# Kernel optimization log

Measured on AMD Instinct MI355X. Metric: run time of the kernel, lower is better.

## Reference

```python
import jax, jax.numpy as jnp
import numpy as np

N1 = 4097
N2 = 8192


def setup_inputs() -> dict:
    key = jax.random.key(0)
    kx, ka, kb, km = jax.random.split(key, 4)
    x = jax.random.normal(kx, ((N1 - 1) * N2 + 1,), dtype=jnp.float32)
    a = jax.random.uniform(ka, (1,), dtype=jnp.float32)
    b = jax.random.uniform(kb, (N2, N1 - 1), dtype=jnp.float32)
    mu = jax.random.uniform(km, (1,), dtype=jnp.float32)
    return {"x": x, "a": a, "b": b, "mu": mu}


def reference(x, a, b, mu):
    n2, n1m1 = b.shape  # (n2, n1-1)
    n1 = n1m1 + 1
    # y = x[1 : (n1-1)*n2 + 1].reshape(n2, n1-1)
    y = x[1:(n1 - 1) * n2 + 1].reshape(n2, n1 - 1)
    # Original loop: i in range(n1-2), j in range(n2-1); term uses y[j, i-1],
    # which at i=0 wraps to the LAST column (negative indexing). Reproduce via roll.
    y_cur = y[: n2 - 1, : n1 - 2]                       # y[j, i]
    y_prev = jnp.roll(y, 1, axis=1)[: n2 - 1, : n1 - 2]  # y[j, i-1] with wraparound
    terms = b[: n2 - 1, : n1 - 2] * (y_cur - y_prev ** 2) ** 2
    return -a * (x[0] - mu) ** 2 - jnp.sum(terms)
```

## Files before the change

kernel.cpp:

```cpp
#include <hip/hip_runtime.h>


#define ROWS  8191
#define BLOCK 256

__global__ __launch_bounds__(BLOCK) void rosen_partial(
    const float* __restrict__ x, const float* __restrict__ b,
    float* __restrict__ partial)
{
    const unsigned r = blockIdx.x;
    const unsigned t = threadIdx.x;
    const size_t   e = (size_t)r * 4096u + (size_t)t * 16u;

    const float4* __restrict__ x4 = (const float4*)(x + e);
    const float4* __restrict__ b4 = (const float4*)(b + e);

    float4 xv0 = x4[0], xv1 = x4[1], xv2 = x4[2], xv3 = x4[3];
    float4 bv0 = b4[0], bv1 = b4[1], bv2 = b4[2], bv3 = b4[3];
    float  xs  = x[e + 16];

    float p0 = (t == 0) ? x[e + 4096] : xv0.x;
    if (t == BLOCK - 1) bv3.w = 0.0f;

    float d, acc;
    d = xv0.y - p0    * p0;     acc  = bv0.x * d * d;
    d = xv0.z - xv0.y * xv0.y;  acc += bv0.y * d * d;
    d = xv0.w - xv0.z * xv0.z;  acc += bv0.z * d * d;
    d = xv1.x - xv0.w * xv0.w;  acc += bv0.w * d * d;
    d = xv1.y - xv1.x * xv1.x;  acc += bv1.x * d * d;
    d = xv1.z - xv1.y * xv1.y;  acc += bv1.y * d * d;
    d = xv1.w - xv1.z * xv1.z;  acc += bv1.z * d * d;
    d = xv2.x - xv1.w * xv1.w;  acc += bv1.w * d * d;
    d = xv2.y - xv2.x * xv2.x;  acc += bv2.x * d * d;
    d = xv2.z - xv2.y * xv2.y;  acc += bv2.y * d * d;
    d = xv2.w - xv2.z * xv2.z;  acc += bv2.z * d * d;
    d = xv3.x - xv2.w * xv2.w;  acc += bv2.w * d * d;
    d = xv3.y - xv3.x * xv3.x;  acc += bv3.x * d * d;
    d = xv3.z - xv3.y * xv3.y;  acc += bv3.y * d * d;
    d = xv3.w - xv3.z * xv3.z;  acc += bv3.z * d * d;
    d = xs    - xv3.w * xv3.w;  acc += bv3.w * d * d;

    #pragma unroll
    for (int off = 32; off > 0; off >>= 1)
        acc += __shfl_down(acc, off, 64);

    __shared__ float s[4];
    const int lane = t & 63;
    const int wid  = t >> 6;
    if (lane == 0) s[wid] = acc;
    __syncthreads();
    if (t == 0)
        partial[r] = s[0] + s[1] + s[2] + s[3];
}

__global__ __launch_bounds__(256) void rosen_final(const float* __restrict__ partial,
                                                   const float* __restrict__ x,
                                                   const float* __restrict__ a,
                                                   const float* __restrict__ mu,
                                                   float* __restrict__ out)
{
    float acc = 0.0f;
    for (int i = threadIdx.x; i < ROWS; i += 256)
        acc += partial[i];

    #pragma unroll
    for (int off = 32; off > 0; off >>= 1)
        acc += __shfl_down(acc, off, 64);

    __shared__ float s[4];
    const int lane = threadIdx.x & 63;
    const int wid  = threadIdx.x >> 6;
    if (lane == 0) s[wid] = acc;
    __syncthreads();
    if (threadIdx.x == 0) {
        float total = s[0] + s[1] + s[2] + s[3];
        float dd = x[0] - mu[0];
        out[0] = -a[0] * dd * dd - total;
    }
}

extern "C" void kernel_launch(void* const* d_in, const int* in_sizes, int n_in,
                              void* d_out, int out_size, void* d_ws, size_t ws_size,
                              hipStream_t stream) {
    const float* x  = (const float*)d_in[0];
    const float* a  = (const float*)d_in[1];
    const float* b  = (const float*)d_in[2];
    const float* mu = (const float*)d_in[3];
    float* out     = (float*)d_out;
    float* partial = (float*)d_ws;

    rosen_partial<<<ROWS, BLOCK, 0, stream>>>(x, b, partial);
    rosen_final<<<1, 256, 0, stream>>>(partial, x, a, mu, out);
}
```

Before: 284.4 us.

## Use a fixed grid with four batched groups per thread

Replaces the one-block-per-row launch (8191 blocks) with 2048 blocks, where each thread covers four 16-element groups spread out by a grid stride. All loads for the four groups are issued before any compute, so more memory requests are in flight per thread. The final reduction shrinks to 2048 partials. In exchange, register use rises (about 128 floats of loads per thread) and occupancy may drop. Each group now needs its own boundary and validity checks.

```diff
diff --git a/kernel.cpp b/kernel.cpp
--- a/kernel.cpp
+++ b/kernel.cpp
@@ -1,56 +1,88 @@
 #include <hip/hip_runtime.h>
 
 
-#define ROWS  8191
-#define BLOCK 256
+#define ROWS     8191u
+#define GROUPS16 (ROWS * 256u)
+#define GRID     2048
+#define BLOCK    256
+#define NTHREAD  ((unsigned)GRID * BLOCK)
+#define ITERS    4
+
+__device__ __forceinline__ float group16(const float4* xv, const float4* bv,
+                                         float p0, float xs, float bw3)
+{
+    float d, s;
+    d = xv[0].y - p0      * p0;       s  = bv[0].x * d * d;
+    d = xv[0].z - xv[0].y * xv[0].y;  s += bv[0].y * d * d;
+    d = xv[0].w - xv[0].z * xv[0].z;  s += bv[0].z * d * d;
+    d = xv[1].x - xv[0].w * xv[0].w;  s += bv[0].w * d * d;
+    d = xv[1].y - xv[1].x * xv[1].x;  s += bv[1].x * d * d;
+    d = xv[1].z - xv[1].y * xv[1].y;  s += bv[1].y * d * d;
+    d = xv[1].w - xv[1].z * xv[1].z;  s += bv[1].z * d * d;
+    d = xv[2].x - xv[1].w * xv[1].w;  s += bv[1].w * d * d;
+    d = xv[2].y - xv[2].x * xv[2].x;  s += bv[2].x * d * d;
+    d = xv[2].z - xv[2].y * xv[2].y;  s += bv[2].y * d * d;
+    d = xv[2].w - xv[2].z * xv[2].z;  s += bv[2].z * d * d;
+    d = xv[3].x - xv[2].w * xv[2].w;  s += bv[2].w * d * d;
+    d = xv[3].y - xv[3].x * xv[3].x;  s += bv[3].x * d * d;
+    d = xv[3].z - xv[3].y * xv[3].y;  s += bv[3].y * d * d;
+    d = xv[3].w - xv[3].z * xv[3].z;  s += bv[3].z * d * d;
+    d = xs      - xv[3].w * xv[3].w;  s += bw3     * d * d;
+    return s;
+}
 
 __global__ __launch_bounds__(BLOCK) void rosen_partial(
     const float* __restrict__ x, const float* __restrict__ b,
     float* __restrict__ partial)
 {
-    const unsigned r = blockIdx.x;
-    const unsigned t = threadIdx.x;
-    const size_t   e = (size_t)r * 4096u + (size_t)t * 16u;
+    const unsigned tid = blockIdx.x * BLOCK + threadIdx.x;
 
-    const float4* __restrict__ x4 = (const float4*)(x + e);
-    const float4* __restrict__ b4 = (const float4*)(b + e);
+    float4   xv[ITERS][4];
+    float4   bv[ITERS][4];
+    float    xs[ITERS];
+    float    xw[ITERS];
+    unsigned c16a[ITERS];
+    bool     vld[ITERS];
 
-    float4 xv0 = x4[0], xv1 = x4[1], xv2 = x4[2], xv3 = x4[3];
-    float4 bv0 = b4[0], bv1 = b4[1], bv2 = b4[2], bv3 = b4[3];
-    float  xs  = x[e + 16];
+    #pragma unroll
+    for (int it = 0; it < ITERS; ++it) {
+        unsigned g  = tid + (unsigned)it * NTHREAD;
+        bool     v  = (g < GROUPS16);
+        unsigned gc = v ? g : (GROUPS16 - 1u);
+        unsigned c16 = gc & 255u;
+        unsigned e   = (gc >> 8) * 4096u + c16 * 16u;
+        vld[it]  = v;
+        c16a[it] = c16;
+        const float4* x4 = (const float4*)(x + e);
+        const float4* b4 = (const float4*)(b + e);
+        xv[it][0] = x4[0]; xv[it][1] = x4[1]; xv[it][2] = x4[2]; xv[it][3] = x4[3];
+        bv[it][0] = b4[0]; bv[it][1] = b4[1]; bv[it][2] = b4[2]; bv[it][3] = b4[3];
+        xs[it] = x[e + 16];
+        float w = 0.0f;
+        if (c16 == 0u) w = x[e + 4096];
+        xw[it] = w;
+    }
 
-    float p0 = (t == 0) ? x[e + 4096] : xv0.x;
-    if (t == BLOCK - 1) bv3.w = 0.0f;
-
-    float d, acc;
-    d = xv0.y - p0    * p0;     acc  = bv0.x * d * d;
-    d = xv0.z - xv0.y * xv0.y;  acc += bv0.y * d * d;
-    d = xv0.w - xv0.z * xv0.z;  acc += bv0.z * d * d;
-    d = xv1.x - xv0.w * xv0.w;  acc += bv0.w * d * d;
-    d = xv1.y - xv1.x * xv1.x;  acc += bv1.x * d * d;
-    d = xv1.z - xv1.y * xv1.y;  acc += bv1.y * d * d;
-    d = xv1.w - xv1.z * xv1.z;  acc += bv1.z * d * d;
-    d = xv2.x - xv1.w * xv1.w;  acc += bv1.w * d * d;
-    d = xv2.y - xv2.x * xv2.x;  acc += bv2.x * d * d;
-    d = xv2.z - xv2.y * xv2.y;  acc += bv2.y * d * d;
-    d = xv2.w - xv2.z * xv2.z;  acc += bv2.z * d * d;
-    d = xv3.x - xv2.w * xv2.w;  acc += bv2.w * d * d;
-    d = xv3.y - xv3.x * xv3.x;  acc += bv3.x * d * d;
-    d = xv3.z - xv3.y * xv3.y;  acc += bv3.y * d * d;
-    d = xv3.w - xv3.z * xv3.z;  acc += bv3.z * d * d;
-    d = xs    - xv3.w * xv3.w;  acc += bv3.w * d * d;
+    float acc = 0.0f;
+    #pragma unroll
+    for (int it = 0; it < ITERS; ++it) {
+        float p0  = (c16a[it] == 0u)   ? xw[it] : xv[it][0].x;
+        float bw3 = (c16a[it] == 255u) ? 0.0f   : bv[it][3].w;
+        float s = group16(&xv[it][0], &bv[it][0], p0, xs[it], bw3);
+        acc += vld[it] ? s : 0.0f;
+    }
 
     #pragma unroll
     for (int off = 32; off > 0; off >>= 1)
         acc += __shfl_down(acc, off, 64);
 
-    __shared__ float s[4];
-    const int lane = t & 63;
-    const int wid  = t >> 6;
-    if (lane == 0) s[wid] = acc;
+    __shared__ float sred[4];
+    const int lane = threadIdx.x & 63;
+    const int wid  = threadIdx.x >> 6;
+    if (lane == 0) sred[wid] = acc;
     __syncthreads();
-    if (t == 0)
-        partial[r] = s[0] + s[1] + s[2] + s[3];
+    if (threadIdx.x == 0)
+        partial[blockIdx.x] = sred[0] + sred[1] + sred[2] + sred[3];
 }
 
 __global__ __launch_bounds__(256) void rosen_final(const float* __restrict__ partial,
@@ -60,20 +92,20 @@
                                                    float* __restrict__ out)
 {
     float acc = 0.0f;
-    for (int i = threadIdx.x; i < ROWS; i += 256)
+    for (int i = threadIdx.x; i < GRID; i += 256)
         acc += partial[i];
 
     #pragma unroll
     for (int off = 32; off > 0; off >>= 1)
         acc += __shfl_down(acc, off, 64);
 
-    __shared__ float s[4];
+    __shared__ float sred[4];
     const int lane = threadIdx.x & 63;
     const int wid  = threadIdx.x >> 6;
-    if (lane == 0) s[wid] = acc;
+    if (lane == 0) sred[wid] = acc;
     __syncthreads();
     if (threadIdx.x == 0) {
-        float total = s[0] + s[1] + s[2] + s[3];
+        float total = sred[0] + sred[1] + sred[2] + sred[3];
         float dd = x[0] - mu[0];
         out[0] = -a[0] * dd * dd - total;
     }
@@ -89,6 +121,6 @@
     float* out     = (float*)d_out;
     float* partial = (float*)d_ws;
 
-    rosen_partial<<<ROWS, BLOCK, 0, stream>>>(x, b, partial);
+    rosen_partial<<<GRID, BLOCK, 0, stream>>>(x, b, partial);
     rosen_final<<<1, 256, 0, stream>>>(partial, x, a, mu, out);
 }
```

Result: faster. 278.7 us (-2.0%).

## Coalesce row loads with lane-strided float4 and loop four rows per block

Applied to the files above, without the earlier changes.

Each wave now loads contiguous float4 chunks across lanes (stride 4 floats per lane) instead of each thread reading 16 contiguous floats, so global accesses are fully coalesced. Neighbor elements across chunk boundaries are obtained via wave shuffles. Each block processes four rows in a loop, cutting the grid from 8191 to 2048 blocks and shrinking the final reduction. The cost is extra shuffle traffic and boundary handling logic, plus less parallelism per row.

```diff
diff --git a/kernel.cpp b/kernel.cpp
--- a/kernel.cpp
+++ b/kernel.cpp
@@ -1,56 +1,80 @@
 #include <hip/hip_runtime.h>
 
 
-#define ROWS  8191
-#define BLOCK 256
+#define ROWS   8191u
+#define GRID   2048
+#define BLOCK  256
+#define ROWSPB 4u
 
 __global__ __launch_bounds__(BLOCK) void rosen_partial(
     const float* __restrict__ x, const float* __restrict__ b,
     float* __restrict__ partial)
 {
-    const unsigned r = blockIdx.x;
-    const unsigned t = threadIdx.x;
-    const size_t   e = (size_t)r * 4096u + (size_t)t * 16u;
+    const unsigned lane = threadIdx.x & 63u;
+    const unsigned w    = threadIdx.x >> 6;
+    float acc = 0.0f;
 
-    const float4* __restrict__ x4 = (const float4*)(x + e);
-    const float4* __restrict__ b4 = (const float4*)(b + e);
+    #pragma unroll 1
+    for (unsigned k = 0; k < ROWSPB; ++k) {
+        const unsigned r = blockIdx.x * ROWSPB + k;
+        if (r >= ROWS) break;
+        const size_t rowoff = (size_t)r * 4096u;
+        const size_t base   = rowoff + w * 1024u + lane * 4u;
 
-    float4 xv0 = x4[0], xv1 = x4[1], xv2 = x4[2], xv3 = x4[3];
-    float4 bv0 = b4[0], bv1 = b4[1], bv2 = b4[2], bv3 = b4[3];
-    float  xs  = x[e + 16];
+        float4 xv0 = *(const float4*)(x + base);
+        float4 xv1 = *(const float4*)(x + base + 256);
+        float4 xv2 = *(const float4*)(x + base + 512);
+        float4 xv3 = *(const float4*)(x + base + 768);
+        float4 bv0 = *(const float4*)(b + base);
+        float4 bv1 = *(const float4*)(b + base + 256);
+        float4 bv2 = *(const float4*)(b + base + 512);
+        float4 bv3 = *(const float4*)(b + base + 768);
 
-    float p0 = (t == 0) ? x[e + 4096] : xv0.x;
-    if (t == BLOCK - 1) bv3.w = 0.0f;
+        float tail = x[rowoff + w * 1024u + 1024u];
+        float wrapv = 0.0f;
+        if (threadIdx.x == 0) wrapv = x[rowoff + 4096u];
+        if (threadIdx.x == BLOCK - 1) bv3.w = 0.0f;
 
-    float d, acc;
-    d = xv0.y - p0    * p0;     acc  = bv0.x * d * d;
-    d = xv0.z - xv0.y * xv0.y;  acc += bv0.y * d * d;
-    d = xv0.w - xv0.z * xv0.z;  acc += bv0.z * d * d;
-    d = xv1.x - xv0.w * xv0.w;  acc += bv0.w * d * d;
-    d = xv1.y - xv1.x * xv1.x;  acc += bv1.x * d * d;
-    d = xv1.z - xv1.y * xv1.y;  acc += bv1.y * d * d;
-    d = xv1.w - xv1.z * xv1.z;  acc += bv1.z * d * d;
-    d = xv2.x - xv1.w * xv1.w;  acc += bv1.w * d * d;
-    d = xv2.y - xv2.x * xv2.x;  acc += bv2.x * d * d;
-    d = xv2.z - xv2.y * xv2.y;  acc += bv2.y * d * d;
-    d = xv2.w - xv2.z * xv2.z;  acc += bv2.z * d * d;
-    d = xv3.x - xv2.w * xv2.w;  acc += bv2.w * d * d;
-    d = xv3.y - xv3.x * xv3.x;  acc += bv3.x * d * d;
-    d = xv3.z - xv3.y * xv3.y;  acc += bv3.y * d * d;
-    d = xv3.w - xv3.z * xv3.z;  acc += bv3.z * d * d;
-    d = xs    - xv3.w * xv3.w;  acc += bv3.w * d * d;
+        float n0 = __shfl_down(xv0.x, 1, 64);
+        float n1 = __shfl_down(xv1.x, 1, 64);
+        float n2 = __shfl_down(xv2.x, 1, 64);
+        float n3 = __shfl_down(xv3.x, 1, 64);
+        float c1 = __shfl(xv1.x, 0, 64);
+        float c2 = __shfl(xv2.x, 0, 64);
+        float c3 = __shfl(xv3.x, 0, 64);
+        if (lane == 63u) { n0 = c1; n1 = c2; n2 = c3; n3 = tail; }
+
+        float pv = xv0.x;
+        if (threadIdx.x == 0) pv = wrapv;
+
+        float d;
+        d = xv0.y - pv    * pv;     acc += bv0.x * d * d;
+        d = xv0.z - xv0.y * xv0.y;  acc += bv0.y * d * d;
+        d = xv0.w - xv0.z * xv0.z;  acc += bv0.z * d * d;
+        d = n0    - xv0.w * xv0.w;  acc += bv0.w * d * d;
+        d = xv1.y - xv1.x * xv1.x;  acc += bv1.x * d * d;
+        d = xv1.z - xv1.y * xv1.y;  acc += bv1.y * d * d;
+        d = xv1.w - xv1.z * xv1.z;  acc += bv1.z * d * d;
+        d = n1    - xv1.w * xv1.w;  acc += bv1.w * d * d;
+        d = xv2.y - xv2.x * xv2.x;  acc += bv2.x * d * d;
+        d = xv2.z - xv2.y * xv2.y;  acc += bv2.y * d * d;
+        d = xv2.w - xv2.z * xv2.z;  acc += bv2.z * d * d;
+        d = n2    - xv2.w * xv2.w;  acc += bv2.w * d * d;
+        d = xv3.y - xv3.x * xv3.x;  acc += bv3.x * d * d;
+        d = xv3.z - xv3.y * xv3.y;  acc += bv3.y * d * d;
+        d = xv3.w - xv3.z * xv3.z;  acc += bv3.z * d * d;
+        d = n3    - xv3.w * xv3.w;  acc += bv3.w * d * d;
+    }
 
     #pragma unroll
     for (int off = 32; off > 0; off >>= 1)
         acc += __shfl_down(acc, off, 64);
 
-    __shared__ float s[4];
-    const int lane = t & 63;
-    const int wid  = t >> 6;
-    if (lane == 0) s[wid] = acc;
+    __shared__ float sred[4];
+    if (lane == 0) sred[w] = acc;
     __syncthreads();
-    if (t == 0)
-        partial[r] = s[0] + s[1] + s[2] + s[3];
+    if (threadIdx.x == 0)
+        partial[blockIdx.x] = sred[0] + sred[1] + sred[2] + sred[3];
 }
 
 __global__ __launch_bounds__(256) void rosen_final(const float* __restrict__ partial,
@@ -60,20 +84,20 @@
                                                    float* __restrict__ out)
 {
     float acc = 0.0f;
-    for (int i = threadIdx.x; i < ROWS; i += 256)
+    for (int i = threadIdx.x; i < GRID; i += 256)
         acc += partial[i];
 
     #pragma unroll
     for (int off = 32; off > 0; off >>= 1)
         acc += __shfl_down(acc, off, 64);
 
-    __shared__ float s[4];
+    __shared__ float sred[4];
     const int lane = threadIdx.x & 63;
     const int wid  = threadIdx.x >> 6;
-    if (lane == 0) s[wid] = acc;
+    if (lane == 0) sred[wid] = acc;
     __syncthreads();
     if (threadIdx.x == 0) {
-        float total = s[0] + s[1] + s[2] + s[3];
+        float total = sred[0] + sred[1] + sred[2] + sred[3];
         float dd = x[0] - mu[0];
         out[0] = -a[0] * dd * dd - total;
     }
@@ -89,6 +113,6 @@
     float* out     = (float*)d_out;
     float* partial = (float*)d_ws;
 
-    rosen_partial<<<ROWS, BLOCK, 0, stream>>>(x, b, partial);
+    rosen_partial<<<GRID, BLOCK, 0, stream>>>(x, b, partial);
     rosen_final<<<1, 256, 0, stream>>>(partial, x, a, mu, out);
 }
```

Result: no change. 283.2 us (-0.4%).
